# Kernel tuning notes

Measured on AMD Instinct MI355X. Metric: run time of the kernel, lower is better.

Reference implementation:

```python
import jax, jax.numpy as jnp
import numpy as np


def setup_inputs() -> dict:
    key = jax.random.key(0)
    ks = jax.random.split(key, 6)
    B, C, H, W = 8, 256, 32, 32
    d = C // 8  # 32
    return {
        "x": jax.random.normal(ks[0], (B, C, H, W), dtype=jnp.float32),
        "Wq": jax.random.normal(ks[1], (d, C), dtype=jnp.float32) * 0.05,
        "bq": jnp.zeros((d,), dtype=jnp.float32),
        "Wk": jax.random.normal(ks[2], (d, C), dtype=jnp.float32) * 0.05,
        "bk": jnp.zeros((d,), dtype=jnp.float32),
        "Wv": jax.random.normal(ks[3], (C, C), dtype=jnp.float32) * 0.05,
        "bv": jnp.zeros((C,), dtype=jnp.float32),
        "Wr": jax.random.normal(ks[4], (d, 2), dtype=jnp.float32) * 0.05,
        "br": jnp.zeros((d,), dtype=jnp.float32),
        "gamma": jnp.array([0.5], dtype=jnp.float32),
    }


def reference(x, Wq, bq, Wk, bk, Wv, bv, Wr, br, gamma):
    B, C, H, W = x.shape
    N = H * W
    d = Wq.shape[0]
    xf = x.reshape(B, C, N)

    # 1x1 convs == per-pixel linear projections
    q = jnp.einsum('dc,bcn->bdn', Wq, xf) + bq[None, :, None]  # (B,d,N)
    k = jnp.einsum('dc,bcn->bdn', Wk, xf) + bk[None, :, None]  # (B,d,N)
    v = jnp.einsum('oc,bcn->bon', Wv, xf) + bv[None, :, None]  # (B,C,N)

    # relative position code: pairwise coord diffs through 1x1 conv (batch-independent)
    gh, gw = jnp.meshgrid(jnp.linspace(0.0, 1.0, H), jnp.linspace(0.0, 1.0, W), indexing='ij')
    coords = jnp.stack([gh.reshape(-1), gw.reshape(-1)])  # (2,N)
    diff = coords[:, :, None] - coords[:, None, :]         # (2,N,N)
    rp_code = jnp.einsum('dt,tij->dij', Wr, diff) + br[:, None, None]  # (d,N,N)

    scale = 1.0 / jnp.sqrt(jnp.asarray(d, dtype=x.dtype))
    score = jnp.einsum('bdi,bdj->bij', q, k) * scale          # (B,N,N)
    rp_score = jnp.einsum('bdi,dij->bij', q, rp_code) * scale  # (B,N,N)
    attn = jax.nn.softmax(score + rp_score, axis=-1)

    # out[b,c,i] = sum_j v[b,c,j] * attn[b,i,j]
    out = jnp.einsum('bcj,bij->bci', v, attn)
    return gamma[0] * out.reshape(B, C, H, W) + x
```

## Files before the change

### kernel.cpp

```cpp
#include <hip/hip_runtime.h>
#include <hip/hip_bf16.h>

#define BATCH 8
#define CH    256
#define NN    1024
#define DD    32

#define QT_OFF 0
#define KT_OFF (BATCH * NN * DD)
#define V_OFF  (2 * BATCH * NN * DD)
#define V2_B   (NN * CH)

#define SCALE_Q (0.17677669529663687f * 1.4426950408889634f)
#define INV31 (1.0f / 31.0f)

typedef __attribute__((ext_vector_type(4))) float f32x4;
typedef __attribute__((ext_vector_type(8))) short bf16x8;

__device__ __forceinline__ unsigned int packbf2(float lo, float hi) {
    __hip_bfloat162 h = __float22bfloat162_rn(make_float2(lo, hi));
    union { __hip_bfloat162 h; unsigned int u; } cv; cv.h = h;
    return cv.u;
}
__device__ __forceinline__ unsigned short f2bf(float x) {
    union { float f; unsigned int u; } v; v.f = x;
    return (unsigned short)((v.u + 0x7FFFu + ((v.u >> 16) & 1u)) >> 16);
}

__global__ __launch_bounds__(256) void proj_kernel(
    const float* __restrict__ x,
    const float* __restrict__ Wq, const float* __restrict__ bq,
    const float* __restrict__ Wk, const float* __restrict__ bk,
    const float* __restrict__ Wv, const float* __restrict__ bv,
    const float* __restrict__ Wr,
    unsigned short* __restrict__ ws)
{
    const int nt   = blockIdx.x;
    const int b    = blockIdx.y;
    const int tid  = threadIdx.x;
    const int wv   = tid >> 6;
    const int lane = tid & 63;
    const int n16  = lane & 15;
    const int q4   = lane >> 4;
    const int n    = nt * 16 + n16;

    f32x4 acc[5];
#pragma unroll
    for (int t = 0; t < 5; t++) acc[t] = (f32x4){0.f, 0.f, 0.f, 0.f};

    const float* wrow[5];
#pragma unroll
    for (int t = 0; t < 5; t++) {
        const int m = (wv * 5 + t) * 16 + n16;
        wrow[t] = (m < 32) ? (Wq + m * CH)
                : (m < 64) ? (Wk + (m - 32) * CH)
                           : (Wv + (m - 64) * CH);
    }

    for (int c0 = 0; c0 < CH; c0 += 32) {
        const int kofs = c0 + q4 * 8;
        float bx[8];
#pragma unroll
        for (int jj = 0; jj < 8; jj++)
            bx[jj] = x[(size_t)(b * CH + kofs + jj) * NN + n];
        union { unsigned int u[4]; bf16x8 v; } bf;
#pragma unroll
        for (int p = 0; p < 4; p++) bf.u[p] = packbf2(bx[2 * p], bx[2 * p + 1]);

#pragma unroll
        for (int t = 0; t < 5; t++) {
            const float* wp = wrow[t] + kofs;
            const float4 a0 = *(const float4*)(wp);
            const float4 a1 = *(const float4*)(wp + 4);
            union { unsigned int u[4]; bf16x8 v; } af;
            af.u[0] = packbf2(a0.x, a0.y); af.u[1] = packbf2(a0.z, a0.w);
            af.u[2] = packbf2(a1.x, a1.y); af.u[3] = packbf2(a1.z, a1.w);
            acc[t] = __builtin_amdgcn_mfma_f32_16x16x32_bf16(af.v, bf.v, acc[t], 0, 0, 0);
        }
    }

    const int jt  = n >> 5;
    const int q4p = (n >> 3) & 3;
    const int jj  = n & 7;
#pragma unroll
    for (int t = 0; t < 5; t++) {
        const int mf = wv * 5 + t;
        const int mb = mf * 16 + q4 * 4;
        if (mb < 32) {
            const float r0 = (acc[t][0] + bq[mb + 0]) * SCALE_Q;
            const float r1 = (acc[t][1] + bq[mb + 1]) * SCALE_Q;
            const float r2 = (acc[t][2] + bq[mb + 2]) * SCALE_Q;
            const float r3 = (acc[t][3] + bq[mb + 3]) * SCALE_Q;
            uint2 st = { packbf2(r0, r1), packbf2(r2, r3) };
            *(uint2*)(ws + QT_OFF + (size_t)(b * NN + n) * DD + mb) = st;
        } else if (mb < 64) {
            const int d = mb - 32;
            const float An = (float)(n >> 5) * INV31;
            const float Bn = (float)(n & 31) * INV31;
            float r[4];
#pragma unroll
            for (int rr = 0; rr < 4; rr++)
                r[rr] = acc[t][rr] + bk[d + rr] - An * Wr[2 * (d + rr)] - Bn * Wr[2 * (d + rr) + 1];
            uint2 st = { packbf2(r[0], r[1]), packbf2(r[2], r[3]) };
            *(uint2*)(ws + KT_OFF + (size_t)(b * NN + n) * DD + d) = st;
        } else {
            const int c = mb - 64;
#pragma unroll
            for (int rr = 0; rr < 4; rr++) {
                const int cc = c + rr;
                const size_t off = V_OFF + (size_t)b * V2_B
                                 + (size_t)jt * 8192 + (size_t)(cc >> 4) * 512
                                 + (size_t)(q4p * 16 + (cc & 15)) * 8 + jj;
                ws[off] = f2bf(acc[t][rr] + bv[cc]);
            }
        }
    }
}

__global__ __launch_bounds__(512) void attn_kernel(
    const float* __restrict__ x,
    const float* __restrict__ gamma,
    const unsigned short* __restrict__ ws,
    float* __restrict__ out)
{
    const int it   = blockIdx.x;
    const int b    = blockIdx.y;
    const int tid  = threadIdx.x;
    const int wv   = (tid >> 6) & 3;
    const int jh   = tid >> 8;
    const int lane = tid & 63;
    const int n    = lane & 15;
    const int q4   = lane >> 4;
    const int i0   = it * 32;
    const int cb   = wv * 64;

    __shared__ float accL[4 * 32 * 64];
    __shared__ float lL[32];

    const unsigned short* qT = ws + QT_OFF + (size_t)b * NN * DD;
    const unsigned short* kT = ws + KT_OFF + (size_t)b * NN * DD + (size_t)jh * 512 * DD;
    const unsigned short* vb = ws + V_OFF + (size_t)b * V2_B
                             + (size_t)jh * 16 * 8192 + (size_t)wv * 4 * 512
                             + (size_t)lane * 8;

    const bf16x8 qf0 = *(const bf16x8*)(qT + (size_t)(i0 + n) * DD + q4 * 8);
    const bf16x8 qf1 = *(const bf16x8*)(qT + (size_t)(i0 + 16 + n) * DD + q4 * 8);

    f32x4 acc0[4], acc1[4];
#pragma unroll
    for (int t = 0; t < 4; t++) {
        acc0[t] = (f32x4){0.f, 0.f, 0.f, 0.f};
        acc1[t] = (f32x4){0.f, 0.f, 0.f, 0.f};
    }
    float lsum0 = 0.f, lsum1 = 0.f;

    bf16x8 ka0 = *(const bf16x8*)(kT + (size_t)(n) * DD + q4 * 8);
    bf16x8 ka1 = *(const bf16x8*)(kT + (size_t)(16 + n) * DD + q4 * 8);
    bf16x8 va[4];
#pragma unroll
    for (int t = 0; t < 4; t++)
        va[t] = *(const bf16x8*)(vb + t * 512);

    const int qh2 = (q4 & 1) * 2;
    int src[4];
#pragma unroll
    for (int t = 0; t < 4; t++) src[t] = (qh2 + (t >> 1)) * 16 + n;

#pragma unroll 4
    for (int ch = 0; ch < 16; ch++) {
        const bf16x8 ka0c = ka0, ka1c = ka1;
        bf16x8 vac[4];
#pragma unroll
        for (int t = 0; t < 4; t++) vac[t] = va[t];

        {
            const int j0 = (ch + 1) * 32;
            ka0 = *(const bf16x8*)(kT + (size_t)(j0 + n) * DD + q4 * 8);
            ka1 = *(const bf16x8*)(kT + (size_t)(j0 + 16 + n) * DD + q4 * 8);
#pragma unroll
            for (int t = 0; t < 4; t++)
                va[t] = *(const bf16x8*)(vb + (ch + 1) * 8192 + t * 512);
        }

        const f32x4 z = {0.f, 0.f, 0.f, 0.f};
        f32x4 s0a = __builtin_amdgcn_mfma_f32_16x16x32_bf16(ka0c, qf0, z, 0, 0, 0);
        f32x4 s1a = __builtin_amdgcn_mfma_f32_16x16x32_bf16(ka1c, qf0, z, 0, 0, 0);
        f32x4 s0b = __builtin_amdgcn_mfma_f32_16x16x32_bf16(ka0c, qf1, z, 0, 0, 0);
        f32x4 s1b = __builtin_amdgcn_mfma_f32_16x16x32_bf16(ka1c, qf1, z, 0, 0, 0);

        float p0a[4], p1a[4], p0b[4], p1b[4];
#pragma unroll
        for (int r = 0; r < 4; r++) {
            p0a[r] = exp2f(s0a[r]);
            p1a[r] = exp2f(s1a[r]);
            p0b[r] = exp2f(s0b[r]);
            p1b[r] = exp2f(s1b[r]);
            lsum0 += p0a[r] + p1a[r];
            lsum1 += p0b[r] + p1b[r];
        }

        unsigned int pk0a[2] = { packbf2(p0a[0], p0a[1]), packbf2(p0a[2], p0a[3]) };
        unsigned int pk1a[2] = { packbf2(p1a[0], p1a[1]), packbf2(p1a[2], p1a[3]) };
        unsigned int pk0b[2] = { packbf2(p0b[0], p0b[1]), packbf2(p0b[2], p0b[3]) };
        unsigned int pk1b[2] = { packbf2(p1b[0], p1b[1]), packbf2(p1b[2], p1b[3]) };
        union { unsigned int u[4]; bf16x8 v; } pfa, pfb;
#pragma unroll
        for (int t = 0; t < 4; t++) {
            const unsigned int loa = (unsigned int)__shfl((int)pk0a[t & 1], src[t], 64);
            const unsigned int hia = (unsigned int)__shfl((int)pk1a[t & 1], src[t], 64);
            const unsigned int lob = (unsigned int)__shfl((int)pk0b[t & 1], src[t], 64);
            const unsigned int hib = (unsigned int)__shfl((int)pk1b[t & 1], src[t], 64);
            pfa.u[t] = (q4 >= 2) ? hia : loa;
            pfb.u[t] = (q4 >= 2) ? hib : lob;
        }

#pragma unroll
        for (int t = 0; t < 4; t++) {
            acc0[t] = __builtin_amdgcn_mfma_f32_16x16x32_bf16(vac[t], pfa.v, acc0[t], 0, 0, 0);
            acc1[t] = __builtin_amdgcn_mfma_f32_16x16x32_bf16(vac[t], pfb.v, acc1[t], 0, 0, 0);
        }
    }

    lsum0 += __shfl_xor(lsum0, 16, 64);
    lsum0 += __shfl_xor(lsum0, 32, 64);
    lsum1 += __shfl_xor(lsum1, 16, 64);
    lsum1 += __shfl_xor(lsum1, 32, 64);

    if (jh == 1) {
#pragma unroll
        for (int t = 0; t < 4; t++)
#pragma unroll
            for (int r = 0; r < 4; r++) {
                accL[(wv * 32 + t * 4 + r) * 64 + lane]      = acc0[t][r];
                accL[(wv * 32 + 16 + t * 4 + r) * 64 + lane] = acc1[t][r];
            }
        if (wv == 0 && lane < 16) lL[lane] = lsum0;
        if (wv == 1 && lane < 16) lL[16 + lane] = lsum1;
    }
    __syncthreads();

    if (jh == 0) {
        const float g = gamma[0];
        const float rl0 = g / (lsum0 + lL[n]);
        const float rl1 = g / (lsum1 + lL[16 + n]);
#pragma unroll
        for (int t = 0; t < 4; t++) {
#pragma unroll
            for (int r = 0; r < 4; r++) {
                const int c = cb + t * 16 + q4 * 4 + r;
                const size_t base = (size_t)(b * CH + c) * NN + i0 + n;
                const float a0 = acc0[t][r] + accL[(wv * 32 + t * 4 + r) * 64 + lane];
                const float a1 = acc1[t][r] + accL[(wv * 32 + 16 + t * 4 + r) * 64 + lane];
                out[base]      = a0 * rl0 + x[base];
                out[base + 16] = a1 * rl1 + x[base + 16];
            }
        }
    }
}

extern "C" void kernel_launch(void* const* d_in, const int* in_sizes, int n_in,
                              void* d_out, int out_size, void* d_ws, size_t ws_size,
                              hipStream_t stream) {
    (void)in_sizes; (void)n_in; (void)out_size; (void)ws_size;
    const float* x     = (const float*)d_in[0];
    const float* Wq    = (const float*)d_in[1];
    const float* bq    = (const float*)d_in[2];
    const float* Wk    = (const float*)d_in[3];
    const float* bk    = (const float*)d_in[4];
    const float* Wv    = (const float*)d_in[5];
    const float* bv    = (const float*)d_in[6];
    const float* Wr    = (const float*)d_in[7];
    const float* gamma = (const float*)d_in[9];
    float* out = (float*)d_out;
    unsigned short* ws = (unsigned short*)d_ws;

    proj_kernel<<<dim3(64, 8), 256, 0, stream>>>(x, Wq, bq, Wk, bk, Wv, bv, Wr, ws);
    attn_kernel<<<dim3(32, 8), 512, 0, stream>>>(x, gamma, ws, out);
}
```

Baseline: 117.7 us.

## Pre-pack weights to bf16 fragment layout and double-buffer K/V prefetch

A new kernel converts the concatenated Wq/Wk/Wv weights to bf16 once per call and stores them in MFMA fragment order in the workspace. The projection kernel then loads each A fragment with a single 16-byte read instead of two float4 loads plus conversion. Separately, the attention loop now prefetches K and V two chunks ahead using a two-slot register buffer rather than one chunk ahead, to hide more load latency. Costs are an extra kernel launch, more workspace, and higher register pressure in the attention kernel; the prefetch at the last iterations reads past the 16 chunks.

```diff
diff --git a/kernel.cpp b/kernel.cpp
--- a/kernel.cpp
+++ b/kernel.cpp
@@ -10,6 +10,7 @@
 #define KT_OFF (BATCH * NN * DD)
 #define V_OFF  (2 * BATCH * NN * DD)
 #define V2_B   (NN * CH)
+#define WF_OFF (V_OFF + BATCH * V2_B)
 
 #define SCALE_Q (0.17677669529663687f * 1.4426950408889634f)
 #define INV31 (1.0f / 31.0f)
@@ -27,12 +28,29 @@
     return (unsigned short)((v.u + 0x7FFFu + ((v.u >> 16) & 1u)) >> 16);
 }
 
+__global__ __launch_bounds__(256) void wrepack_kernel(
+    const float* __restrict__ Wq, const float* __restrict__ Wk,
+    const float* __restrict__ Wv, unsigned short* __restrict__ ws)
+{
+    const int gid = blockIdx.x * 256 + threadIdx.x;
+    const int e = gid * 4;
+    const int m = e >> 8;
+    const int k = e & 255;
+    const float* src = (m < 32) ? (Wq + m * CH + k)
+                     : (m < 64) ? (Wk + (m - 32) * CH + k)
+                                : (Wv + (m - 64) * CH + k);
+    const float4 w = *(const float4*)src;
+    const int mf = m >> 4, kc = k >> 5;
+    const int lf = ((k >> 3) & 3) * 16 + (m & 15);
+    const int jj = k & 7;
+    uint2 st = { packbf2(w.x, w.y), packbf2(w.z, w.w) };
+    *(uint2*)(ws + WF_OFF + ((size_t)(mf * 8 + kc) * 64 + lf) * 8 + jj) = st;
+}
+
 __global__ __launch_bounds__(256) void proj_kernel(
     const float* __restrict__ x,
-    const float* __restrict__ Wq, const float* __restrict__ bq,
-    const float* __restrict__ Wk, const float* __restrict__ bk,
-    const float* __restrict__ Wv, const float* __restrict__ bv,
-    const float* __restrict__ Wr,
+    const float* __restrict__ bq, const float* __restrict__ bk,
+    const float* __restrict__ bv, const float* __restrict__ Wr,
     unsigned short* __restrict__ ws)
 {
     const int nt   = blockIdx.x;
@@ -48,17 +66,10 @@
 #pragma unroll
     for (int t = 0; t < 5; t++) acc[t] = (f32x4){0.f, 0.f, 0.f, 0.f};
 
-    const float* wrow[5];
-#pragma unroll
-    for (int t = 0; t < 5; t++) {
-        const int m = (wv * 5 + t) * 16 + n16;
-        wrow[t] = (m < 32) ? (Wq + m * CH)
-                : (m < 64) ? (Wk + (m - 32) * CH)
-                           : (Wv + (m - 64) * CH);
-    }
-
-    for (int c0 = 0; c0 < CH; c0 += 32) {
-        const int kofs = c0 + q4 * 8;
+    const unsigned short* wfl = ws + WF_OFF + (size_t)lane * 8;
+
+    for (int kc = 0; kc < 8; kc++) {
+        const int kofs = kc * 32 + q4 * 8;
         float bx[8];
 #pragma unroll
         for (int jj = 0; jj < 8; jj++)
@@ -69,13 +80,8 @@
 
 #pragma unroll
         for (int t = 0; t < 5; t++) {
-            const float* wp = wrow[t] + kofs;
-            const float4 a0 = *(const float4*)(wp);
-            const float4 a1 = *(const float4*)(wp + 4);
-            union { unsigned int u[4]; bf16x8 v; } af;
-            af.u[0] = packbf2(a0.x, a0.y); af.u[1] = packbf2(a0.z, a0.w);
-            af.u[2] = packbf2(a1.x, a1.y); af.u[3] = packbf2(a1.z, a1.w);
-            acc[t] = __builtin_amdgcn_mfma_f32_16x16x32_bf16(af.v, bf.v, acc[t], 0, 0, 0);
+            const bf16x8 af = *(const bf16x8*)(wfl + (size_t)((wv * 5 + t) * 8 + kc) * 512);
+            acc[t] = __builtin_amdgcn_mfma_f32_16x16x32_bf16(af, bf.v, acc[t], 0, 0, 0);
         }
     }
 
@@ -154,12 +160,17 @@
     }
     float lsum0 = 0.f, lsum1 = 0.f;
 
-    bf16x8 ka0 = *(const bf16x8*)(kT + (size_t)(n) * DD + q4 * 8);
-    bf16x8 ka1 = *(const bf16x8*)(kT + (size_t)(16 + n) * DD + q4 * 8);
-    bf16x8 va[4];
-#pragma unroll
-    for (int t = 0; t < 4; t++)
-        va[t] = *(const bf16x8*)(vb + t * 512);
+    bf16x8 kaS[2][2];
+    bf16x8 vaS[2][4];
+#pragma unroll
+    for (int s = 0; s < 2; s++) {
+        const int j0 = s * 32;
+        kaS[s][0] = *(const bf16x8*)(kT + (size_t)(j0 + n) * DD + q4 * 8);
+        kaS[s][1] = *(const bf16x8*)(kT + (size_t)(j0 + 16 + n) * DD + q4 * 8);
+#pragma unroll
+        for (int t = 0; t < 4; t++)
+            vaS[s][t] = *(const bf16x8*)(vb + s * 8192 + t * 512);
+    }
 
     const int qh2 = (q4 & 1) * 2;
     int src[4];
@@ -168,18 +179,19 @@
 
 #pragma unroll 4
     for (int ch = 0; ch < 16; ch++) {
-        const bf16x8 ka0c = ka0, ka1c = ka1;
+        const int st = ch & 1;
+        const bf16x8 ka0c = kaS[st][0], ka1c = kaS[st][1];
         bf16x8 vac[4];
 #pragma unroll
-        for (int t = 0; t < 4; t++) vac[t] = va[t];
+        for (int t = 0; t < 4; t++) vac[t] = vaS[st][t];
 
         {
-            const int j0 = (ch + 1) * 32;
-            ka0 = *(const bf16x8*)(kT + (size_t)(j0 + n) * DD + q4 * 8);
-            ka1 = *(const bf16x8*)(kT + (size_t)(j0 + 16 + n) * DD + q4 * 8);
+            const int j0 = (ch + 2) * 32;
+            kaS[st][0] = *(const bf16x8*)(kT + (size_t)(j0 + n) * DD + q4 * 8);
+            kaS[st][1] = *(const bf16x8*)(kT + (size_t)(j0 + 16 + n) * DD + q4 * 8);
 #pragma unroll
             for (int t = 0; t < 4; t++)
-                va[t] = *(const bf16x8*)(vb + (ch + 1) * 8192 + t * 512);
+                vaS[st][t] = *(const bf16x8*)(vb + (ch + 2) * 8192 + t * 512);
         }
 
         const f32x4 z = {0.f, 0.f, 0.f, 0.f};
@@ -274,6 +286,7 @@
     float* out = (float*)d_out;
     unsigned short* ws = (unsigned short*)d_ws;
 
-    proj_kernel<<<dim3(64, 8), 256, 0, stream>>>(x, Wq, bq, Wk, bk, Wv, bv, Wr, ws);
+    wrepack_kernel<<<80, 256, 0, stream>>>(Wq, Wk, Wv, ws);
+    proj_kernel<<<dim3(64, 8), 256, 0, stream>>>(x, bq, bk, bv, Wr, ws);
     attn_kernel<<<dim3(32, 8), 512, 0, stream>>>(x, gamma, ws, out);
 }
```

After: 114.4 us. -2.8%, faster.
